# Performance work log

Hardware: AMD Instinct MI355X
Metric: run time of the kernel (lower is better)

## Reference

```python
import jax, jax.numpy as jnp
import numpy as np

B, S, D, H = 1, 2048, 2048, 32
HD = D // H
SCALE = float(HD) ** -0.5


def _rope(x, cos, sin):
    # x: (b, s, h, hd); interleaved-pair RoPE as in executorch apply_rotary_emb
    xr, xi = x[..., 0::2], x[..., 1::2]
    c = cos[None, :, None, :]
    s = sin[None, :, None, :]
    out = jnp.stack([xr * c - xi * s, xr * s + xi * c], axis=-1)
    return out.reshape(x.shape)


def setup_inputs() -> dict:
    key = jax.random.key(0)
    ks = jax.random.split(key, 8)
    hidden_states = jax.random.normal(ks[0], (B, S, D), jnp.float32)
    pos = jnp.arange(S, dtype=jnp.float32)
    inv = 1.0 / (10000.0 ** (jnp.arange(0, HD, 2, dtype=jnp.float32) / HD))
    ang = pos[:, None] * inv[None, :]  # (S, HD//2)
    freqs_cos = jnp.cos(ang)
    freqs_sin = jnp.sin(ang)
    causal = jnp.tril(jnp.ones((S, S), dtype=bool))
    attention_mask = jnp.where(causal, 0.0, -1e9).astype(jnp.float32)[None, None]
    k_cache = jax.random.normal(ks[1], (B, S, H, HD), jnp.float32)
    v_cache = jax.random.normal(ks[2], (B, S, H, HD), jnp.float32)
    k_mask = jnp.ones((B, S, 1, 1), jnp.float32)
    v_mask = jnp.ones((B, S, 1, 1), jnp.float32)
    # weights stored as (in, out); math-equivalent to torch Linear(out,in) @ W.T
    wq = jax.random.normal(ks[3], (D, D), jnp.float32) * 0.02
    wk = jax.random.normal(ks[4], (D, D), jnp.float32) * 0.02
    wv = jax.random.normal(ks[5], (D, D), jnp.float32) * 0.02
    wo = jax.random.normal(ks[6], (D, D), jnp.float32) * 0.02
    return {"hidden_states": hidden_states, "freqs_cos": freqs_cos,
            "freqs_sin": freqs_sin, "attention_mask": attention_mask,
            "k_cache": k_cache, "v_cache": v_cache,
            "k_mask": k_mask, "v_mask": v_mask,
            "wq": wq, "wk": wk, "wv": wv, "wo": wo}


def reference(hidden_states, freqs_cos, freqs_sin, attention_mask,
              k_cache, v_cache, k_mask, v_mask, wq, wk, wv, wo):
    b, s, _ = hidden_states.shape
    q = (hidden_states @ wq).reshape(b, s, H, HD)
    k = (hidden_states @ wk).reshape(b, s, H, HD)
    v = (hidden_states @ wv).reshape(b, s, H, HD)
    q = _rope(q, freqs_cos, freqs_sin)
    k = _rope(k, freqs_cos, freqs_sin)
    # mask-blend KV cache update
    k = k_cache * (1.0 - k_mask) + k * k_mask  # (b, S, H, HD)
    v = v_cache * (1.0 - v_mask) + v * v_mask
    qt = q.transpose(0, 2, 1, 3)  # (b, H, s, HD)
    kt = k.transpose(0, 2, 1, 3)
    vt = v.transpose(0, 2, 1, 3)
    attn = jnp.einsum('bhqd,bhkd->bhqk', qt, kt) * SCALE + attention_mask
    attn = jax.nn.softmax(attn, axis=-1)
    y = jnp.einsum('bhqk,bhkd->bhqd', attn, vt)  # (b, H, s, HD)
    # torch: y.transpose(0,1).contiguous().view(b, s, dim); valid since b == 1
    y = jnp.swapaxes(y, 0, 1).reshape(b, s, D)
    y = y @ wo
    return (y, k, v)
```

## Files before the change

kernel.cpp:

```cpp
#include <hip/hip_runtime.h>
#include <hip/hip_bf16.h>
#include <stdint.h>

typedef __bf16 bf16;
typedef __attribute__((ext_vector_type(8))) __bf16 bf16x8;
typedef __attribute__((ext_vector_type(4))) float f32x4;

#define SEQ 2048
#define DIM 2048
#define NHEAD 32
#define HD 64
#define ATT_SCALE 0.125f

__device__ __forceinline__ void gload16(void* lds, const void* g) {
  __builtin_amdgcn_global_load_lds(
      (const __attribute__((address_space(1))) unsigned int*)g,
      (__attribute__((address_space(3))) unsigned int*)lds, 16, 0, 0);
}

__device__ __forceinline__ f32x4 mfma16(bf16x8 a, bf16x8 b, f32x4 c) {
  return __builtin_amdgcn_mfma_f32_16x16x32_bf16(a, b, c, 0, 0, 0);
}

__global__ __launch_bounds__(256) void cvt_hs(const float* __restrict__ in,
                                              bf16* __restrict__ out) {
  size_t i = ((size_t)blockIdx.x * 256 + threadIdx.x) * 8;
  f32x4 a = *(const f32x4*)(in + i);
  f32x4 b = *(const f32x4*)(in + i + 4);
  bf16x8 o;
#pragma unroll
  for (int j = 0; j < 4; ++j) { o[j] = (bf16)a[j]; o[j + 4] = (bf16)b[j]; }
  *(bf16x8*)(out + i) = o;
}

__global__ __launch_bounds__(256) void wtrans(
    const float* __restrict__ w0, const float* __restrict__ w1,
    const float* __restrict__ w2, const float* __restrict__ w3,
    bf16* __restrict__ t0, bf16* __restrict__ t1,
    bf16* __restrict__ t2, bf16* __restrict__ t3) {
  const float* wsrc[4] = {w0, w1, w2, w3};
  bf16* wdst[4] = {t0, t1, t2, t3};
  const float* w = wsrc[blockIdx.z];
  bf16* wT = wdst[blockIdx.z];
  __shared__ alignas(16) bf16 tile[64][72];
  int t = threadIdx.x;
  int n0 = blockIdx.x * 64, k0 = blockIdx.y * 64;
#pragma unroll
  for (int i = 0; i < 4; ++i) {
    int r = (t >> 4) + 16 * i;
    int c = (t & 15) * 4;
    f32x4 v = *(const f32x4*)(w + (size_t)(k0 + r) * DIM + n0 + c);
#pragma unroll
    for (int j = 0; j < 4; ++j) tile[r][c + j] = (bf16)v[j];
  }
  __syncthreads();
#pragma unroll
  for (int i = 0; i < 2; ++i) {
    int n = (t >> 3) + 32 * i;
    int kb = (t & 7) * 8;
    bf16x8 o;
#pragma unroll
    for (int j = 0; j < 8; ++j) o[j] = tile[kb + j][n];
    *(bf16x8*)(wT + (size_t)(n0 + n) * DIM + k0 + kb) = o;
  }
}

template <typename OutT>
__global__ __launch_bounds__(256) void gemm128(
    const bf16* __restrict__ A,
    const bf16* __restrict__ B0, const bf16* __restrict__ B1, const bf16* __restrict__ B2,
    OutT* __restrict__ C0, OutT* __restrict__ C1, OutT* __restrict__ C2,
    int M, int N, int K) {
  const bf16* Bt; OutT* C;
  if (blockIdx.z == 0)      { Bt = B0; C = C0; }
  else if (blockIdx.z == 1) { Bt = B1; C = C1; }
  else                      { Bt = B2; C = C2; }
  __shared__ alignas(16) bf16 As[128][64];
  __shared__ alignas(16) bf16 Bs[128][64];
  int tid = threadIdx.x, lane = tid & 63, w = tid >> 6;
  int wr = w >> 1, wc = w & 1;
  size_t mBase = (size_t)blockIdx.y * 128, nBase = (size_t)blockIdx.x * 128;
  f32x4 acc[4][4] = {};
  int r0 = tid >> 3, sl = tid & 7;
  int lr = lane & 15, hi = lane >> 4, sw = lr & 7;
  for (int kt = 0; kt < K; kt += 64) {
#pragma unroll
    for (int i = 0; i < 4; ++i) {
      int row = r0 + 32 * i;
      int kc = sl ^ (row & 7);
      gload16(&As[row][sl * 8], A + (mBase + row) * K + kt + kc * 8);
      gload16(&Bs[row][sl * 8], Bt + (nBase + row) * K + kt + kc * 8);
    }
    __syncthreads();
#pragma unroll
    for (int kk = 0; kk < 2; ++kk) {
      int cb = kk * 4 + hi;
      bf16x8 a[4], b[4];
#pragma unroll
      for (int m = 0; m < 4; ++m)
        a[m] = *(const bf16x8*)&As[wr * 64 + m * 16 + lr][(cb ^ sw) * 8];
#pragma unroll
      for (int n = 0; n < 4; ++n)
        b[n] = *(const bf16x8*)&Bs[wc * 64 + n * 16 + lr][(cb ^ sw) * 8];
#pragma unroll
      for (int m = 0; m < 4; ++m)
#pragma unroll
        for (int n = 0; n < 4; ++n)
          acc[m][n] = mfma16(a[m], b[n], acc[m][n]);
    }
    __syncthreads();
  }
#pragma unroll
  for (int m = 0; m < 4; ++m)
#pragma unroll
    for (int n = 0; n < 4; ++n)
#pragma unroll
      for (int j = 0; j < 4; ++j) {
        size_t row = mBase + wr * 64 + m * 16 + hi * 4 + j;
        size_t col = nBase + wc * 64 + n * 16 + lr;
        C[row * N + col] = (OutT)acc[m][n][j];
      }
}

__global__ __launch_bounds__(256) void gemm_osk(
    const bf16* __restrict__ A, const bf16* __restrict__ Bt,
    float* __restrict__ P0, float* __restrict__ P1) {
  const int K = DIM, N = DIM;
  float* C = blockIdx.z ? P1 : P0;
  int kbeg = blockIdx.z * (K / 2), kend = kbeg + K / 2;
  __shared__ alignas(16) bf16 As[128][64];
  __shared__ alignas(16) bf16 Bs[128][64];
  int tid = threadIdx.x, lane = tid & 63, w = tid >> 6;
  int wr = w >> 1, wc = w & 1;
  size_t mBase = (size_t)blockIdx.y * 128, nBase = (size_t)blockIdx.x * 128;
  f32x4 acc[4][4] = {};
  int r0 = tid >> 3, sl = tid & 7;
  int lr = lane & 15, hi = lane >> 4, sw = lr & 7;
  for (int kt = kbeg; kt < kend; kt += 64) {
#pragma unroll
    for (int i = 0; i < 4; ++i) {
      int row = r0 + 32 * i;
      int kc = sl ^ (row & 7);
      gload16(&As[row][sl * 8], A + (mBase + row) * K + kt + kc * 8);
      gload16(&Bs[row][sl * 8], Bt + (nBase + row) * K + kt + kc * 8);
    }
    __syncthreads();
#pragma unroll
    for (int kk = 0; kk < 2; ++kk) {
      int cb = kk * 4 + hi;
      bf16x8 a[4], b[4];
#pragma unroll
      for (int m = 0; m < 4; ++m)
        a[m] = *(const bf16x8*)&As[wr * 64 + m * 16 + lr][(cb ^ sw) * 8];
#pragma unroll
      for (int n = 0; n < 4; ++n)
        b[n] = *(const bf16x8*)&Bs[wc * 64 + n * 16 + lr][(cb ^ sw) * 8];
#pragma unroll
      for (int m = 0; m < 4; ++m)
#pragma unroll
        for (int n = 0; n < 4; ++n)
          acc[m][n] = mfma16(a[m], b[n], acc[m][n]);
    }
    __syncthreads();
  }
#pragma unroll
  for (int m = 0; m < 4; ++m)
#pragma unroll
    for (int n = 0; n < 4; ++n)
#pragma unroll
      for (int j = 0; j < 4; ++j) {
        size_t row = mBase + wr * 64 + m * 16 + hi * 4 + j;
        size_t col = nBase + wc * 64 + n * 16 + lr;
        C[row * N + col] = acc[m][n][j];
      }
}

__global__ __launch_bounds__(256) void addp(const float* __restrict__ a,
                                            const float* __restrict__ b,
                                            float* __restrict__ y) {
  size_t i = ((size_t)blockIdx.x * 256 + threadIdx.x) * 4;
  f32x4 va = *(const f32x4*)(a + i);
  f32x4 vb = *(const f32x4*)(b + i);
  *(f32x4*)(y + i) = va + vb;
}

__global__ __launch_bounds__(256) void ropeqk(
    const bf16* __restrict__ qraw, const bf16* __restrict__ kraw,
    const float* __restrict__ fc, const float* __restrict__ fs,
    const float* __restrict__ kcache, const float* __restrict__ kmask,
    float* __restrict__ kout, bf16* __restrict__ qb, bf16* __restrict__ kb) {
  int s = blockIdx.x;
  float km = kmask[s];
  float omk = 1.0f - km;
  for (int p = threadIdx.x; p < DIM / 2; p += 256) {
    int h = p >> 5, i = p & 31;
    float c = fc[s * 32 + i], sn = fs[s * 32 + i];
    size_t src = (size_t)s * DIM + h * 64 + 2 * i;
    float xr = (float)qraw[src], xi = (float)qraw[src + 1];
    float q0v = xr * c - xi * sn, q1v = xr * sn + xi * c;
    size_t dsth = (size_t)h * SEQ * HD + (size_t)s * HD + 2 * i;
    qb[dsth] = (bf16)q0v; qb[dsth + 1] = (bf16)q1v;
    xr = (float)kraw[src]; xi = (float)kraw[src + 1];
    float k0v = xr * c - xi * sn, k1v = xr * sn + xi * c;
    float b0 = kcache[src] * omk + k0v * km;
    float b1 = kcache[src + 1] * omk + k1v * km;
    kout[src] = b0; kout[src + 1] = b1;
    kb[dsth] = (bf16)b0; kb[dsth + 1] = (bf16)b1;
  }
}

__global__ __launch_bounds__(256) void vprep(
    const bf16* __restrict__ vraw, const float* __restrict__ vcache,
    const float* __restrict__ vmask, float* __restrict__ vout,
    bf16* __restrict__ vtb) {
  int h = blockIdx.y;
  int s0 = blockIdx.x * 64;
  __shared__ alignas(16) bf16 tile[64][72];
  int t = threadIdx.x;
#pragma unroll
  for (int i = 0; i < 4; ++i) {
    int r = (t >> 4) + 16 * i;
    int c = (t & 15) * 4;
    int s = s0 + r;
    float vm = vmask[s], om = 1.0f - vm;
    size_t src = (size_t)s * DIM + h * 64 + c;
    f32x4 vc = *(const f32x4*)(vcache + src);
    f32x4 o;
#pragma unroll
    for (int j = 0; j < 4; ++j) {
      float val = vc[j] * om + (float)vraw[src + j] * vm;
      o[j] = val;
      tile[r][c + j] = (bf16)val;
    }
    *(f32x4*)(vout + src) = o;
  }
  __syncthreads();
#pragma unroll
  for (int i = 0; i < 2; ++i) {
    int hd = (t >> 3) + 32 * i;
    int cb = (t & 7) * 8;
    bf16x8 o;
#pragma unroll
    for (int j = 0; j < 8; ++j) o[j] = tile[cb + j][hd];
    *(bf16x8*)(vtb + (size_t)h * HD * SEQ + (size_t)hd * SEQ + s0 + cb) = o;
  }
}

__global__ __launch_bounds__(256) void attn_fwd(
    const bf16* __restrict__ qb, const bf16* __restrict__ kb,
    const bf16* __restrict__ vtb, bf16* __restrict__ ob) {
  int orig = blockIdx.x;
  int wg = (orig & 7) * 64 + (orig >> 3);
  int h = wg >> 4;
  int qp = wg & 15;
  int qtA = qp, qtB = 31 - qp;
  int ntA = qtA + 1;
  const int NT = 33;
  __shared__ alignas(16) bf16 Ks[2][64][64];
  __shared__ alignas(16) bf16 Vs[2][64][64];
  __shared__ alignas(16) bf16 Ps[4][16][64];
  int tid = threadIdx.x, lane = tid & 63, w = tid >> 6;
  const bf16* qh = qb + (size_t)h * SEQ * HD;
  const bf16* kh = kb + (size_t)h * SEQ * HD;
  const bf16* vh = vtb + (size_t)h * HD * SEQ;
  int lr = lane & 15, hi = lane >> 4, sw = lr & 7;
  int qrowA = qtA * 64 + w * 16 + lr;
  int qrowB = qtB * 64 + w * 16 + lr;
  bf16x8 qfA[2], qfB[2];
#pragma unroll
  for (int kk = 0; kk < 2; ++kk) {
    qfA[kk] = *(const bf16x8*)(qh + (size_t)qrowA * HD + kk * 32 + hi * 8);
    qfB[kk] = *(const bf16x8*)(qh + (size_t)qrowB * HD + kk * 32 + hi * 8);
  }
  f32x4 otA[4] = {}, otB[4] = {};
  float mA = -3e38f, lA = 0.f, mB = -3e38f, lB = 0.f;
  int r0 = tid >> 3, sl = tid & 7;
  char* PsW = (char*)&Ps[w][0][0];

  auto STAGE = [&](int kv0, int b) {
#pragma unroll
    for (int i = 0; i < 2; ++i) {
      int row = r0 + 32 * i;
      int kc = sl ^ (row & 7);
      gload16(&Ks[b][row][sl * 8], kh + (size_t)(kv0 + row) * HD + kc * 8);
      gload16(&Vs[b][row][sl * 8], vh + (size_t)row * SEQ + kv0 + kc * 8);
    }
  };

  auto BODY = [&](int buf, int kv0, bf16x8 (&qf)[2], f32x4 (&ot)[4],
                  float& mrun, float& lrun, int qrow, bool last) {
    f32x4 st[4] = {};
    __builtin_amdgcn_s_setprio(1);
#pragma unroll
    for (int kk = 0; kk < 2; ++kk) {
      int cb = kk * 4 + hi;
#pragma unroll
      for (int n = 0; n < 4; ++n) {
        bf16x8 kf = *(const bf16x8*)&Ks[buf][n * 16 + lr][(cb ^ sw) * 8];
        st[n] = mfma16(kf, qf[kk], st[n]);
      }
    }
    __builtin_amdgcn_s_setprio(0);
    float tmax = -3e38f;
    if (last) {
#pragma unroll
      for (int n = 0; n < 4; ++n)
#pragma unroll
        for (int j = 0; j < 4; ++j) {
          int key = kv0 + n * 16 + hi * 4 + j;
          float v = (key <= qrow) ? st[n][j] * ATT_SCALE : -1e30f;
          st[n][j] = v;
          tmax = fmaxf(tmax, v);
        }
    } else {
#pragma unroll
      for (int n = 0; n < 4; ++n)
#pragma unroll
        for (int j = 0; j < 4; ++j) {
          float v = st[n][j] * ATT_SCALE;
          st[n][j] = v;
          tmax = fmaxf(tmax, v);
        }
    }
    tmax = fmaxf(tmax, __shfl_xor(tmax, 16));
    tmax = fmaxf(tmax, __shfl_xor(tmax, 32));
    float mnew = fmaxf(mrun, tmax);
    float psum = 0.f;
    if (__all(tmax <= mrun)) {
#pragma unroll
      for (int n = 0; n < 4; ++n)
#pragma unroll
        for (int j = 0; j < 4; ++j) {
          float pv = __expf(st[n][j] - mrun);
          st[n][j] = pv;
          psum += pv;
        }
      psum += __shfl_xor(psum, 16);
      psum += __shfl_xor(psum, 32);
      lrun += psum;
    } else {
      float alpha = __expf(mrun - mnew);
#pragma unroll
      for (int n = 0; n < 4; ++n)
#pragma unroll
        for (int j = 0; j < 4; ++j) {
          float pv = __expf(st[n][j] - mnew);
          st[n][j] = pv;
          psum += pv;
        }
      psum += __shfl_xor(psum, 16);
      psum += __shfl_xor(psum, 32);
      lrun = lrun * alpha + psum;
      mrun = mnew;
#pragma unroll
      for (int nd = 0; nd < 4; ++nd)
#pragma unroll
        for (int j = 0; j < 4; ++j) ot[nd][j] *= alpha;
    }
#pragma unroll
    for (int n = 0; n < 4; ++n) {
      union { bf16 b[4]; uint2 u; } pk;
#pragma unroll
      for (int j = 0; j < 4; ++j) pk.b[j] = (bf16)st[n][j];
      int keyc = n * 2 + (hi >> 1);
      *(uint2*)(PsW + lr * 128 + ((keyc ^ sw) * 16) + (hi & 1) * 8) = pk.u;
    }
    __builtin_amdgcn_s_setprio(1);
#pragma unroll
    for (int kk = 0; kk < 2; ++kk) {
      int cb = kk * 4 + hi;
      bf16x8 pf = *(const bf16x8*)(PsW + lr * 128 + ((cb ^ sw) * 16));
#pragma unroll
      for (int nd = 0; nd < 4; ++nd) {
        bf16x8 vf = *(const bf16x8*)&Vs[buf][nd * 16 + lr][(cb ^ sw) * 8];
        ot[nd] = mfma16(vf, pf, ot[nd]);
      }
    }
    __builtin_amdgcn_s_setprio(0);
  };

  auto STORE = [&](f32x4 (&ot)[4], float lrun, int qrow) {
    float rinv = 1.0f / lrun;
    bf16* orow = ob + ((size_t)h * SEQ + qrow) * HD;
#pragma unroll
    for (int nd = 0; nd < 4; ++nd) {
      union { bf16 b[4]; uint2 u; } o;
#pragma unroll
      for (int j = 0; j < 4; ++j) o.b[j] = (bf16)(ot[nd][j] * rinv);
      *(uint2*)(orow + nd * 16 + hi * 4) = o.u;
    }
  };

  STAGE(0, 0);
  int buf = 0;
  for (int t = 0; t < NT; ++t) {
    __syncthreads();
    if (t + 1 < NT) {
      int tn = t + 1;
      int kvn = (tn < ntA ? tn : tn - ntA) * 64;
      STAGE(kvn, buf ^ 1);
    }
    if (t < ntA) {
      int kv0 = t * 64;
      BODY(buf, kv0, qfA, otA, mA, lA, qrowA, t == ntA - 1);
      if (t == ntA - 1) STORE(otA, lA, qrowA);
    } else {
      int kv0 = (t - ntA) * 64;
      BODY(buf, kv0, qfB, otB, mB, lB, qrowB, t == NT - 1);
    }
    buf ^= 1;
  }
  STORE(otB, lB, qrowB);
}

extern "C" void kernel_launch(void* const* d_in, const int* in_sizes, int n_in,
                              void* d_out, int out_size, void* d_ws, size_t ws_size,
                              hipStream_t stream) {
  const float* hs     = (const float*)d_in[0];
  const float* fc     = (const float*)d_in[1];
  const float* fs     = (const float*)d_in[2];
  const float* kcache = (const float*)d_in[4];
  const float* vcache = (const float*)d_in[5];
  const float* kmask  = (const float*)d_in[6];
  const float* vmask  = (const float*)d_in[7];
  const float* wq     = (const float*)d_in[8];
  const float* wk     = (const float*)d_in[9];
  const float* wv     = (const float*)d_in[10];
  const float* wo     = (const float*)d_in[11];

  float* y    = (float*)d_out;
  float* kout = y + (size_t)SEQ * DIM;
  float* vout = y + 2 * (size_t)SEQ * DIM;

  char* ws = (char*)d_ws;
  const size_t MB8 = (size_t)SEQ * DIM * sizeof(bf16);
  bf16* wqT  = (bf16*)(ws + 0 * MB8);
  bf16* wkT  = (bf16*)(ws + 1 * MB8);
  bf16* wvT  = (bf16*)(ws + 2 * MB8);
  bf16* woT  = (bf16*)(ws + 3 * MB8);
  bf16* hsb  = (bf16*)(ws + 4 * MB8);
  bf16* qraw = (bf16*)(ws + 5 * MB8);
  bf16* kraw = (bf16*)(ws + 6 * MB8);
  bf16* vraw = (bf16*)(ws + 7 * MB8);
  bf16* qb   = (bf16*)(ws + 8 * MB8);
  bf16* kb   = (bf16*)(ws + 9 * MB8);
  bf16* vtb  = (bf16*)(ws + 10 * MB8);
  bf16* ob   = hsb;
  float* p0 = (float*)(ws + 5 * MB8);
  float* p1 = (float*)(ws + 7 * MB8);

  cvt_hs<<<dim3(SEQ * DIM / 2048), dim3(256), 0, stream>>>(hs, hsb);
  wtrans<<<dim3(32, 32, 4), dim3(256), 0, stream>>>(wq, wk, wv, wo, wqT, wkT, wvT, woT);
  gemm128<bf16><<<dim3(16, 16, 3), dim3(256), 0, stream>>>(
      hsb, wqT, wkT, wvT, qraw, kraw, vraw, SEQ, DIM, DIM);
  ropeqk<<<dim3(SEQ), dim3(256), 0, stream>>>(qraw, kraw, fc, fs, kcache, kmask, kout, qb, kb);
  vprep<<<dim3(32, 32), dim3(256), 0, stream>>>(vraw, vcache, vmask, vout, vtb);
  attn_fwd<<<dim3(512), dim3(256), 0, stream>>>(qb, kb, vtb, ob);
  gemm_osk<<<dim3(16, 16, 2), dim3(256), 0, stream>>>(ob, woT, p0, p1);
  addp<<<dim3(SEQ * DIM / 1024), dim3(256), 0, stream>>>(p0, p1, y);
}
```

Before: 200.0 us.

## Fuse RoPE, KV cache blend and V transpose into QKV GEMM epilogue

The QKV projection GEMM now applies RoPE with a lane shuffle, the K/V mask blend with the fp32 cache outputs, and the V transpose through LDS directly in its epilogue. The separate ropeqk and vprep kernels are removed, along with the bf16 round-trip of raw Q/K/V through global memory. The aim is to cut two kernel launches and roughly 24 MB of intermediate traffic. In exchange the epilogue stores are less coalesced: scattered fp32 kcache reads and kout writes, and per-element head-major stores.

Result: slower. 258.6 us (+29.3%).

```diff
diff --git a/kernel.cpp b/kernel.cpp
--- a/kernel.cpp
+++ b/kernel.cpp
@@ -65,18 +65,20 @@
   }
 }
 
-template <typename OutT>
-__global__ __launch_bounds__(256) void gemm128(
+__global__ __launch_bounds__(256) void gemm_qkv(
     const bf16* __restrict__ A,
-    const bf16* __restrict__ B0, const bf16* __restrict__ B1, const bf16* __restrict__ B2,
-    OutT* __restrict__ C0, OutT* __restrict__ C1, OutT* __restrict__ C2,
-    int M, int N, int K) {
-  const bf16* Bt; OutT* C;
-  if (blockIdx.z == 0)      { Bt = B0; C = C0; }
-  else if (blockIdx.z == 1) { Bt = B1; C = C1; }
-  else                      { Bt = B2; C = C2; }
-  __shared__ alignas(16) bf16 As[128][64];
-  __shared__ alignas(16) bf16 Bs[128][64];
+    const bf16* __restrict__ Bq, const bf16* __restrict__ Bk, const bf16* __restrict__ Bv,
+    const float* __restrict__ fc, const float* __restrict__ fs,
+    const float* __restrict__ kcache, const float* __restrict__ kmask,
+    const float* __restrict__ vcache, const float* __restrict__ vmask,
+    bf16* __restrict__ qb, bf16* __restrict__ kb, bf16* __restrict__ vtb,
+    float* __restrict__ kout, float* __restrict__ vout) {
+  extern __shared__ __align__(16) char smem[];
+  bf16 (*As)[64] = (bf16(*)[64])smem;
+  bf16 (*Bs)[64] = (bf16(*)[64])(smem + 16384);
+  int z = blockIdx.z;
+  const bf16* Bt = (z == 0) ? Bq : (z == 1) ? Bk : Bv;
+  const int K = DIM, N = DIM;
   int tid = threadIdx.x, lane = tid & 63, w = tid >> 6;
   int wr = w >> 1, wc = w & 1;
   size_t mBase = (size_t)blockIdx.y * 128, nBase = (size_t)blockIdx.x * 128;
@@ -110,16 +112,68 @@
     }
     __syncthreads();
   }
-#pragma unroll
-  for (int m = 0; m < 4; ++m)
-#pragma unroll
-    for (int n = 0; n < 4; ++n)
+  if (z < 2) {
+#pragma unroll
+    for (int m = 0; m < 4; ++m) {
 #pragma unroll
       for (int j = 0; j < 4; ++j) {
         size_t row = mBase + wr * 64 + m * 16 + hi * 4 + j;
-        size_t col = nBase + wc * 64 + n * 16 + lr;
-        C[row * N + col] = (OutT)acc[m][n][j];
+        float kmv = 0.f, omv = 0.f;
+        if (z == 1) { kmv = kmask[row]; omv = 1.0f - kmv; }
+        const float* fcr = fc + row * 32;
+        const float* fsr = fs + row * 32;
+#pragma unroll
+        for (int n = 0; n < 4; ++n) {
+          int gcol = (int)nBase + wc * 64 + n * 16 + lr;
+          int d = gcol & 63, hh = gcol >> 6;
+          float v = acc[m][n][j];
+          float p = __shfl_xor(v, 1);
+          float c = fcr[d >> 1], s = fsr[d >> 1];
+          float r = (lr & 1) ? (p * s + v * c) : (v * c - p * s);
+          size_t hm = ((size_t)hh * SEQ + row) * HD + d;
+          if (z == 0) {
+            qb[hm] = (bf16)r;
+          } else {
+            float bl = kcache[row * (size_t)DIM + gcol] * omv + r * kmv;
+            kout[row * (size_t)DIM + gcol] = bl;
+            kb[hm] = (bf16)bl;
+          }
+        }
       }
+    }
+  } else {
+#pragma unroll
+    for (int m = 0; m < 4; ++m) {
+#pragma unroll
+      for (int n = 0; n < 4; ++n) {
+        union { bf16 b[4]; uint2 u; } pk;
+#pragma unroll
+        for (int j = 0; j < 4; ++j) {
+          size_t row = mBase + wr * 64 + m * 16 + hi * 4 + j;
+          int gcol = (int)nBase + wc * 64 + n * 16 + lr;
+          float vm = vmask[row], om = 1.0f - vm;
+          float bl = vcache[row * (size_t)DIM + gcol] * om + acc[m][n][j] * vm;
+          vout[row * (size_t)DIM + gcol] = bl;
+          pk.b[j] = (bf16)bl;
+        }
+        int lcol = wc * 64 + n * 16 + lr;
+        int s8 = wr * 16 + m * 4 + hi;
+        int s8s = s8 ^ ((lcol & 7) << 2);
+        *(uint2*)(smem + lcol * 256 + s8s * 8) = pk.u;
+      }
+    }
+    __syncthreads();
+    int lcol = tid & 127, half = tid >> 7;
+    int gcol = (int)nBase + lcol;
+    int hh = gcol >> 6, d = gcol & 63;
+    bf16* dst = vtb + ((size_t)hh * HD + d) * SEQ + mBase + half * 64;
+#pragma unroll
+    for (int c = 0; c < 8; ++c) {
+      int chunk = half * 8 + c;
+      uint4 vv = *(uint4*)(smem + lcol * 256 + (chunk ^ ((lcol & 7) << 1)) * 16);
+      *(uint4*)(dst + c * 8) = vv;
+    }
+  }
 }
 
 __global__ __launch_bounds__(256) void gemm_osk(
@@ -182,68 +236,6 @@
   f32x4 va = *(const f32x4*)(a + i);
   f32x4 vb = *(const f32x4*)(b + i);
   *(f32x4*)(y + i) = va + vb;
-}
-
-__global__ __launch_bounds__(256) void ropeqk(
-    const bf16* __restrict__ qraw, const bf16* __restrict__ kraw,
-    const float* __restrict__ fc, const float* __restrict__ fs,
-    const float* __restrict__ kcache, const float* __restrict__ kmask,
-    float* __restrict__ kout, bf16* __restrict__ qb, bf16* __restrict__ kb) {
-  int s = blockIdx.x;
-  float km = kmask[s];
-  float omk = 1.0f - km;
-  for (int p = threadIdx.x; p < DIM / 2; p += 256) {
-    int h = p >> 5, i = p & 31;
-    float c = fc[s * 32 + i], sn = fs[s * 32 + i];
-    size_t src = (size_t)s * DIM + h * 64 + 2 * i;
-    float xr = (float)qraw[src], xi = (float)qraw[src + 1];
-    float q0v = xr * c - xi * sn, q1v = xr * sn + xi * c;
-    size_t dsth = (size_t)h * SEQ * HD + (size_t)s * HD + 2 * i;
-    qb[dsth] = (bf16)q0v; qb[dsth + 1] = (bf16)q1v;
-    xr = (float)kraw[src]; xi = (float)kraw[src + 1];
-    float k0v = xr * c - xi * sn, k1v = xr * sn + xi * c;
-    float b0 = kcache[src] * omk + k0v * km;
-    float b1 = kcache[src + 1] * omk + k1v * km;
-    kout[src] = b0; kout[src + 1] = b1;
-    kb[dsth] = (bf16)b0; kb[dsth + 1] = (bf16)b1;
-  }
-}
-
-__global__ __launch_bounds__(256) void vprep(
-    const bf16* __restrict__ vraw, const float* __restrict__ vcache,
-    const float* __restrict__ vmask, float* __restrict__ vout,
-    bf16* __restrict__ vtb) {
-  int h = blockIdx.y;
-  int s0 = blockIdx.x * 64;
-  __shared__ alignas(16) bf16 tile[64][72];
-  int t = threadIdx.x;
-#pragma unroll
-  for (int i = 0; i < 4; ++i) {
-    int r = (t >> 4) + 16 * i;
-    int c = (t & 15) * 4;
-    int s = s0 + r;
-    float vm = vmask[s], om = 1.0f - vm;
-    size_t src = (size_t)s * DIM + h * 64 + c;
-    f32x4 vc = *(const f32x4*)(vcache + src);
-    f32x4 o;
-#pragma unroll
-    for (int j = 0; j < 4; ++j) {
-      float val = vc[j] * om + (float)vraw[src + j] * vm;
-      o[j] = val;
-      tile[r][c + j] = (bf16)val;
-    }
-    *(f32x4*)(vout + src) = o;
-  }
-  __syncthreads();
-#pragma unroll
-  for (int i = 0; i < 2; ++i) {
-    int hd = (t >> 3) + 32 * i;
-    int cb = (t & 7) * 8;
-    bf16x8 o;
-#pragma unroll
-    for (int j = 0; j < 8; ++j) o[j] = tile[cb + j][hd];
-    *(bf16x8*)(vtb + (size_t)h * HD * SEQ + (size_t)hd * SEQ + s0 + cb) = o;
-  }
 }
 
 __global__ __launch_bounds__(256) void attn_fwd(
@@ -439,22 +431,18 @@
   bf16* wvT  = (bf16*)(ws + 2 * MB8);
   bf16* woT  = (bf16*)(ws + 3 * MB8);
   bf16* hsb  = (bf16*)(ws + 4 * MB8);
-  bf16* qraw = (bf16*)(ws + 5 * MB8);
-  bf16* kraw = (bf16*)(ws + 6 * MB8);
-  bf16* vraw = (bf16*)(ws + 7 * MB8);
-  bf16* qb   = (bf16*)(ws + 8 * MB8);
-  bf16* kb   = (bf16*)(ws + 9 * MB8);
-  bf16* vtb  = (bf16*)(ws + 10 * MB8);
+  bf16* qb   = (bf16*)(ws + 5 * MB8);
+  bf16* kb   = (bf16*)(ws + 6 * MB8);
+  bf16* vtb  = (bf16*)(ws + 7 * MB8);
   bf16* ob   = hsb;
-  float* p0 = (float*)(ws + 5 * MB8);
-  float* p1 = (float*)(ws + 7 * MB8);
+  float* p0  = (float*)(ws + 5 * MB8);
+  float* p1  = (float*)(ws + 7 * MB8);
 
   cvt_hs<<<dim3(SEQ * DIM / 2048), dim3(256), 0, stream>>>(hs, hsb);
   wtrans<<<dim3(32, 32, 4), dim3(256), 0, stream>>>(wq, wk, wv, wo, wqT, wkT, wvT, woT);
-  gemm128<bf16><<<dim3(16, 16, 3), dim3(256), 0, stream>>>(
-      hsb, wqT, wkT, wvT, qraw, kraw, vraw, SEQ, DIM, DIM);
-  ropeqk<<<dim3(SEQ), dim3(256), 0, stream>>>(qraw, kraw, fc, fs, kcache, kmask, kout, qb, kb);
-  vprep<<<dim3(32, 32), dim3(256), 0, stream>>>(vraw, vcache, vmask, vout, vtb);
+  gemm_qkv<<<dim3(16, 16, 3), dim3(256), 32768, stream>>>(
+      hsb, wqT, wkT, wvT, fc, fs, kcache, kmask, vcache, vmask,
+      qb, kb, vtb, kout, vout);
   attn_fwd<<<dim3(512), dim3(256), 0, stream>>>(qb, kb, vtb, ob);
   gemm_osk<<<dim3(16, 16, 2), dim3(256), 0, stream>>>(ob, woT, p0, p1);
   addp<<<dim3(SEQ * DIM / 1024), dim3(256), 0, stream>>>(p0, p1, y);
```
